# Optimization experiments

Measured on AMD Instinct MI355X. Metric: run time of the kernel, lower is better.

## Reference

```python
import jax, jax.numpy as jnp
import numpy as np

D = 1024   # embedding_dim
H = 16     # head_num
DH = D // H
STD = 0.02


def setup_inputs() -> dict:
    key = jax.random.key(0)
    ks = jax.random.split(key, 8)
    B, S = 16, 2048
    inp = {
        "hidden_states": jax.random.normal(ks[0], (B, S, D), dtype=jnp.float32),
        "attention_mask": jnp.zeros((B, 1, S), dtype=jnp.float32),
        # nn.Linear params, stored as [in, out] for direct matmul
        "Wq": jax.random.normal(ks[1], (D, D), dtype=jnp.float32) * STD,
        "bq": jnp.zeros((D,), dtype=jnp.float32),
        "Wqa": jax.random.normal(ks[2], (D, H), dtype=jnp.float32) * STD,
        "bqa": jnp.zeros((H,), dtype=jnp.float32),
        "Wk": jax.random.normal(ks[3], (D, D), dtype=jnp.float32) * STD,
        "bk": jnp.zeros((D,), dtype=jnp.float32),
        "Wka": jax.random.normal(ks[4], (D, H), dtype=jnp.float32) * STD,
        "bka": jnp.zeros((H,), dtype=jnp.float32),
        "Wt": jax.random.normal(ks[5], (D, D), dtype=jnp.float32) * STD,
        "bt": jnp.zeros((D,), dtype=jnp.float32),
    }
    return inp


def reference(hidden_states, attention_mask, Wq, bq, Wqa, bqa, Wk, bk, Wka, bka, Wt, bt):
    B, S, _ = hidden_states.shape
    scale = 1.0 / np.sqrt(DH).astype(np.float32)

    mixed_q = hidden_states @ Wq + bq          # [B,S,D]
    mixed_k = hidden_states @ Wk + bk          # [B,S,D]

    # per-head query pooling scores: [B,S,H] -> [B,H,S]
    q_score = jnp.transpose(mixed_q @ Wqa + bqa, (0, 2, 1)) * scale + attention_mask
    q_weight = jax.nn.softmax(q_score, axis=-1)                 # [B,H,S]

    q_layer = mixed_q.reshape(B, S, H, DH).transpose(0, 2, 1, 3)  # [B,H,S,dh]
    pooled_q = jnp.einsum('bhs,bhsd->bhd', q_weight, q_layer)     # [B,H,dh]
    pooled_q_flat = pooled_q.reshape(B, 1, D)                     # [B,1,D] (head-major)

    # elementwise modulate keys with pooled query (broadcast, no repeat)
    mixed_qk = mixed_k * pooled_q_flat                            # [B,S,D]

    qk_score = jnp.transpose(mixed_qk @ Wka + bka, (0, 2, 1)) * scale + attention_mask
    qk_weight = jax.nn.softmax(qk_score, axis=-1)                 # [B,H,S]

    k_layer = mixed_qk.reshape(B, S, H, DH).transpose(0, 2, 1, 3)  # [B,H,S,dh]
    pooled_k = jnp.einsum('bhs,bhsd->bhd', qk_weight, k_layer)     # [B,H,dh]

    weighted = pooled_k[:, :, None, :] * q_layer                   # [B,H,S,dh]
    weighted = weighted.transpose(0, 2, 1, 3).reshape(B, S, D)     # [B,S,D]

    return weighted @ Wt + bt + mixed_q
```

## Files before the change

### kernel.cpp

```cpp
#include <hip/hip_runtime.h>
#include <hip/hip_bf16.h>
#include <stdint.h>

#define D_ 1024
#define H_ 16
#define DH_ 64
#define S_ 2048
#define B_ 16
static constexpr float SCALE = 0.125f;

typedef __bf16 bf16_t;
typedef __bf16 bf16x8 __attribute__((ext_vector_type(8)));
typedef __bf16 bf16x4 __attribute__((ext_vector_type(4)));
typedef float  f32x4  __attribute__((ext_vector_type(4)));

__device__ __forceinline__ void llds16(const void* g, void* l) {
  __builtin_amdgcn_global_load_lds(
      (const __attribute__((address_space(1))) void*)g,
      (__attribute__((address_space(3))) void*)l, 16, 0, 0);
}

__global__ __launch_bounds__(256)
void f32_to_bf16(const float* __restrict__ src, bf16_t* __restrict__ dst) {
  size_t base = ((size_t)blockIdx.x * 256 + threadIdx.x) * 8;
  f32x4 a = *(const f32x4*)&src[base];
  f32x4 b = *(const f32x4*)&src[base + 4];
  bf16x8 o;
#pragma unroll
  for (int i = 0; i < 4; ++i) { o[i] = (bf16_t)a[i]; o[4 + i] = (bf16_t)b[i]; }
  *(bf16x8*)&dst[base] = o;
}

__global__ __launch_bounds__(256)
void transpose1024(const float* __restrict__ src, bf16_t* __restrict__ dst) {
  __shared__ bf16_t t[64][65];
  const int n0 = blockIdx.x * 64, k0 = blockIdx.y * 64;
  const int r = threadIdx.x >> 4, c4 = (threadIdx.x & 15) * 4;
#pragma unroll
  for (int p = 0; p < 4; ++p) {
    int row = p * 16 + r;
    f32x4 f = *(const f32x4*)&src[(size_t)(k0 + row) * 1024 + n0 + c4];
#pragma unroll
    for (int i = 0; i < 4; ++i) t[row][c4 + i] = (bf16_t)f[i];
  }
  __syncthreads();
#pragma unroll
  for (int p = 0; p < 4; ++p) {
    int row = p * 16 + r;
    bf16x4 v;
#pragma unroll
    for (int i = 0; i < 4; ++i) v[i] = t[c4 + i][row];
    *(bf16x4*)&dst[(size_t)(n0 + row) * 1024 + k0 + c4] = v;
  }
}

__global__ __launch_bounds__(256)
void transpose_small(const float* __restrict__ src, bf16_t* __restrict__ dst) {
  int k = blockIdx.x * 256 + threadIdx.x;
  if (k < 1024) {
#pragma unroll
    for (int h = 0; h < H_; ++h) dst[h * 1024 + k] = (bf16_t)src[k * H_ + h];
  }
}

__global__ __launch_bounds__(256)
void conv_misc(const float* bqa, const float* bka, const float* mask,
               bf16_t* obqa, bf16_t* obka, bf16_t* omask) {
  int i = blockIdx.x * 256 + threadIdx.x;
  const float* src; bf16_t* dst; int off;
  if      (i < 16)    { src = bqa;  dst = obqa;  off = i; }
  else if (i < 32)    { src = bka;  dst = obka;  off = i - 16; }
  else if (i < 32800) { src = mask; dst = omask; off = i - 32; }
  else return;
  dst[off] = (bf16_t)src[off];
}

template <int MODE>
__global__ __launch_bounds__(512, 1)
void gemm256(const bf16_t* __restrict__ A, const bf16_t* __restrict__ BT,
             const float* __restrict__ bias, void* __restrict__ Cout,
             const float* __restrict__ pscale, const bf16_t* __restrict__ resid) {
  constexpr int K = 1024;
  __shared__ __align__(16) bf16_t lds[2][2][256 * 64];
  const int tid = threadIdx.x;
  const int lane = tid & 63, wid = tid >> 6;
  const int wm = wid >> 2, wn = wid & 3;

  const int wgid = (blockIdx.x & 7) * 64 + (blockIdx.x >> 3);
  const int m0 = (wgid >> 2) * 256;
  const int n0 = (wgid & 3) * 256;

  const bf16_t* gA[4];
  const bf16_t* gB[4];
  int ldsOff[4];
#pragma unroll
  for (int i = 0; i < 4; ++i) {
    int c = i * 512 + tid;
    int r = c >> 3, j = c & 7;
    int col = ((j ^ (r & 7)) << 3);
    gA[i] = A  + (size_t)(m0 + r) * K + col;
    gB[i] = BT + (size_t)(n0 + r) * K + col;
    ldsOff[i] = c * 8;
  }

  f32x4 acc[8][4] = {};
  const int ar = lane & 15;
  const int kq = lane >> 4;

  bf16_t* curA = &lds[0][0][0]; bf16_t* curB = &lds[0][1][0];
  bf16_t* nxtA = &lds[1][0][0]; bf16_t* nxtB = &lds[1][1][0];

#pragma unroll
  for (int i = 0; i < 4; ++i) { llds16(gA[i], curA + ldsOff[i]); llds16(gB[i], curB + ldsOff[i]); }
  __syncthreads();

  for (int t = 0; t < 16; ++t) {
    const int koff = (t + 1) * 64;
#pragma unroll
    for (int q = 0; q < 4; ++q) {
      if (t < 15) {
        llds16(gA[q] + koff, nxtA + ldsOff[q]);
        llds16(gB[q] + koff, nxtB + ldsOff[q]);
      }
      const int mh = q >> 1, nh = q & 1;
      bf16x8 af[4][2], bg[2][2];
#pragma unroll
      for (int mm = 0; mm < 4; ++mm) {
        int r = wm * 128 + (mh * 4 + mm) * 16 + ar;
#pragma unroll
        for (int kk = 0; kk < 2; ++kk)
          af[mm][kk] = *(const bf16x8*)&curA[r * 64 + (((kk * 4 + kq) ^ (r & 7)) << 3)];
      }
#pragma unroll
      for (int nn = 0; nn < 2; ++nn) {
        int r = wn * 64 + (nh * 2 + nn) * 16 + ar;
#pragma unroll
        for (int kk = 0; kk < 2; ++kk)
          bg[nn][kk] = *(const bf16x8*)&curB[r * 64 + (((kk * 4 + kq) ^ (r & 7)) << 3)];
      }
      __builtin_amdgcn_s_barrier();
      __builtin_amdgcn_s_setprio(1);
#pragma unroll
      for (int mm = 0; mm < 4; ++mm)
#pragma unroll
        for (int nn = 0; nn < 2; ++nn)
#pragma unroll
          for (int kk = 0; kk < 2; ++kk)
            acc[mh * 4 + mm][nh * 2 + nn] = __builtin_amdgcn_mfma_f32_16x16x32_bf16(
                af[mm][kk], bg[nn][kk], acc[mh * 4 + mm][nh * 2 + nn], 0, 0, 0);
      __builtin_amdgcn_s_setprio(0);
      if (q < 3) __builtin_amdgcn_s_barrier();
    }
    __syncthreads();
    bf16_t* tA = curA; curA = nxtA; nxtA = tA;
    bf16_t* tB = curB; curB = nxtB; nxtB = tB;
  }

  float* st = (float*)(&lds[0][0][0]) + wid * (16 * 68);
  const int b = m0 / S_;
  const int erow = lane >> 2;
  const int ecol = (lane & 3) * 16;
  const int gcb = n0 + wn * 64;
  const int qrow = (lane >> 4) * 4;
  const int qcol = lane & 15;
  f32x4 bb[4], ps[4];
#pragma unroll
  for (int q = 0; q < 4; ++q) bb[q] = *(const f32x4*)&bias[gcb + ecol + q * 4];
  if (MODE == 1) {
#pragma unroll
    for (int q = 0; q < 4; ++q) ps[q] = *(const f32x4*)&pscale[b * D_ + gcb + ecol + q * 4];
  }
#pragma unroll
  for (int m = 0; m < 8; ++m) {
#pragma unroll
    for (int n = 0; n < 4; ++n)
#pragma unroll
      for (int j = 0; j < 4; ++j)
        st[(qrow + j) * 68 + n * 16 + qcol] = acc[m][n][j];
    asm volatile("s_waitcnt lgkmcnt(0)" ::: "memory");
    __builtin_amdgcn_sched_barrier(0);
    const int grow = m0 + wm * 128 + m * 16 + erow;
    f32x4 v[4];
#pragma unroll
    for (int q = 0; q < 4; ++q) v[q] = *(f32x4*)&st[erow * 68 + ecol + q * 4];
#pragma unroll
    for (int q = 0; q < 4; ++q)
#pragma unroll
      for (int i = 0; i < 4; ++i) v[q][i] += bb[q][i];
    if (MODE == 1) {
#pragma unroll
      for (int q = 0; q < 4; ++q)
#pragma unroll
        for (int i = 0; i < 4; ++i) v[q][i] *= ps[q][i];
    }
    if (MODE == 2) {
      bf16x8 r0 = *(const bf16x8*)&resid[(size_t)grow * D_ + gcb + ecol];
      bf16x8 r1 = *(const bf16x8*)&resid[(size_t)grow * D_ + gcb + ecol + 8];
#pragma unroll
      for (int i = 0; i < 4; ++i) { v[0][i] += (float)r0[i]; v[1][i] += (float)r0[4 + i]; }
#pragma unroll
      for (int i = 0; i < 4; ++i) { v[2][i] += (float)r1[i]; v[3][i] += (float)r1[4 + i]; }
      float* op = (float*)Cout + (size_t)grow * D_ + gcb + ecol;
#pragma unroll
      for (int q = 0; q < 4; ++q) *(f32x4*)&op[q * 4] = v[q];
    } else {
      bf16x8 o0, o1;
#pragma unroll
      for (int i = 0; i < 4; ++i) { o0[i] = (bf16_t)v[0][i]; o0[4 + i] = (bf16_t)v[1][i]; }
#pragma unroll
      for (int i = 0; i < 4; ++i) { o1[i] = (bf16_t)v[2][i]; o1[4 + i] = (bf16_t)v[3][i]; }
      bf16_t* op = (bf16_t*)Cout + (size_t)grow * D_ + gcb + ecol;
      *(bf16x8*)&op[0] = o0;
      *(bf16x8*)&op[8] = o1;
    }
  }
}

__global__ __launch_bounds__(256)
void score_kernel(const bf16_t* __restrict__ X, const bf16_t* __restrict__ WaT,
                  const bf16_t* __restrict__ ba, const bf16_t* __restrict__ mask,
                  float* __restrict__ scores) {
  const int lane = threadIdx.x & 63, wid = threadIdx.x >> 6;
  const int m0 = blockIdx.x * 64 + wid * 16;
  const int ar = lane & 15, ak = (lane >> 4) * 8;
  f32x4 acc = {};
  for (int k0 = 0; k0 < D_; k0 += 32) {
    bf16x8 a = *(const bf16x8*)&X[(size_t)(m0 + ar) * D_ + k0 + ak];
    bf16x8 b = *(const bf16x8*)&WaT[(size_t)ar * D_ + k0 + ak];
    acc = __builtin_amdgcn_mfma_f32_16x16x32_bf16(a, b, acc, 0, 0, 0);
  }
  const int h = lane & 15;
  const int srow = m0 + (lane >> 4) * 4;
  const int bb = srow / S_;
  const int s0 = srow - bb * S_;
  const float bah = (float)ba[h];
  f32x4 outv;
#pragma unroll
  for (int j = 0; j < 4; ++j)
    outv[j] = (acc[j] + bah) * SCALE + (float)mask[(size_t)bb * S_ + s0 + j];
  *(f32x4*)&scores[((size_t)(bb * H_ + h)) * S_ + s0] = outv;
}

__global__ __launch_bounds__(256)
void softmax_rows(const float* __restrict__ scores, float* __restrict__ wout) {
  __shared__ float rA[4], rB[4];
  const int tid = threadIdx.x, lane = tid & 63, wid = tid >> 6;
  const float* srow = scores + (size_t)blockIdx.x * S_;
  float* wrow = wout + (size_t)blockIdx.x * S_;
  f32x4 v0 = *(const f32x4*)&srow[tid * 4];
  f32x4 v1 = *(const f32x4*)&srow[1024 + tid * 4];
  float mx = fmaxf(fmaxf(fmaxf(v0[0], v0[1]), fmaxf(v0[2], v0[3])),
                   fmaxf(fmaxf(v1[0], v1[1]), fmaxf(v1[2], v1[3])));
#pragma unroll
  for (int o = 32; o; o >>= 1) mx = fmaxf(mx, __shfl_xor(mx, o));
  if (lane == 0) rA[wid] = mx;
  __syncthreads();
  mx = fmaxf(fmaxf(rA[0], rA[1]), fmaxf(rA[2], rA[3]));
  float sum = 0.f;
#pragma unroll
  for (int i = 0; i < 4; ++i) { v0[i] = __expf(v0[i] - mx); sum += v0[i]; }
#pragma unroll
  for (int i = 0; i < 4; ++i) { v1[i] = __expf(v1[i] - mx); sum += v1[i]; }
#pragma unroll
  for (int o = 32; o; o >>= 1) sum += __shfl_xor(sum, o);
  if (lane == 0) rB[wid] = sum;
  __syncthreads();
  sum = rB[0] + rB[1] + rB[2] + rB[3];
  const float inv = 1.0f / sum;
#pragma unroll
  for (int i = 0; i < 4; ++i) { v0[i] *= inv; v1[i] *= inv; }
  *(f32x4*)&wrow[tid * 4] = v0;
  *(f32x4*)&wrow[1024 + tid * 4] = v1;
}

__global__ __launch_bounds__(256)
void pool_partial(const bf16_t* __restrict__ X, const float* __restrict__ w,
                  float* __restrict__ partials) {
  __shared__ float sm[2][1024];
  const int tid = threadIdx.x;
  const int chunk = blockIdx.x, b = blockIdx.y;
  const int s0 = chunk * 32;
  const int dc = (tid & 127) * 8;
  const int sp = tid >> 7;
  const int h = dc >> 6;
  const float* wrow = w + ((size_t)b * H_ + h) * S_ + s0;
  const bf16_t* Xb = X + ((size_t)b * S_ + s0) * D_ + dc;
  float acc[8] = {};
  for (int s = sp; s < 32; s += 2) {
    bf16x8 xv = *(const bf16x8*)&Xb[(size_t)s * D_];
    float wt = wrow[s];
#pragma unroll
    for (int j = 0; j < 8; ++j) acc[j] += wt * (float)xv[j];
  }
#pragma unroll
  for (int j = 0; j < 8; ++j) sm[sp][dc + j] = acc[j];
  __syncthreads();
  const int d0 = tid * 4;
  f32x4 r;
#pragma unroll
  for (int j = 0; j < 4; ++j) r[j] = sm[0][d0 + j] + sm[1][d0 + j];
  *(f32x4*)&partials[((size_t)chunk * B_ + b) * D_ + d0] = r;
}

__global__ __launch_bounds__(256)
void pool_reduce(const float* __restrict__ partials, float* __restrict__ pooled) {
  const int idx = blockIdx.x * 256 + threadIdx.x;
  float s = 0.f;
#pragma unroll 8
  for (int c = 0; c < 64; ++c) s += partials[(size_t)c * (B_ * D_) + idx];
  pooled[idx] = s;
}

__global__ __launch_bounds__(256)
void weighted_kernel(const bf16_t* __restrict__ mq, const float* __restrict__ pk,
                     bf16_t* __restrict__ out) {
  size_t idx = ((size_t)blockIdx.x * 256 + threadIdx.x) * 8;
  int d0 = (int)(idx & (D_ - 1));
  int b = (int)(idx >> 21);
  bf16x8 v = *(const bf16x8*)&mq[idx];
  const float* pkb = pk + (size_t)b * D_ + d0;
  bf16x8 o;
#pragma unroll
  for (int i = 0; i < 8; ++i) o[i] = (bf16_t)((float)v[i] * pkb[i]);
  *(bf16x8*)&out[idx] = o;
}

extern "C" void kernel_launch(void* const* d_in, const int* in_sizes, int n_in,
                              void* d_out, int out_size, void* d_ws, size_t ws_size,
                              hipStream_t stream) {
  const float* hs   = (const float*)d_in[0];
  const float* mask = (const float*)d_in[1];
  const float* Wq   = (const float*)d_in[2];
  const float* bq   = (const float*)d_in[3];
  const float* Wqa  = (const float*)d_in[4];
  const float* bqa  = (const float*)d_in[5];
  const float* Wk   = (const float*)d_in[6];
  const float* bk   = (const float*)d_in[7];
  const float* Wka  = (const float*)d_in[8];
  const float* bka  = (const float*)d_in[9];
  const float* Wt   = (const float*)d_in[10];
  const float* bt   = (const float*)d_in[11];

  char* ws = (char*)d_ws;
  float*  pq    = (float*)(ws + (64u << 10));
  float*  pk    = (float*)(ws + (128u << 10));
  bf16_t* bqac  = (bf16_t*)(ws + (192u << 10));
  bf16_t* bkac  = (bf16_t*)(ws + (192u << 10) + 64);
  bf16_t* maskc = (bf16_t*)(ws + (256u << 10));
  bf16_t* WqaT  = (bf16_t*)(ws + (1u << 20));
  bf16_t* WkaT  = (bf16_t*)(ws + (1u << 20) + 32768);
  bf16_t* WqT   = (bf16_t*)(ws + (2u << 20));
  bf16_t* WkT   = (bf16_t*)(ws + (4u << 20));
  bf16_t* WtT   = (bf16_t*)(ws + (6u << 20));
  bf16_t* hsb   = (bf16_t*)(ws + (8u << 20));
  bf16_t* mq    = (bf16_t*)(ws + (8u << 20) + ((size_t)64 << 20));
  bf16_t* mqk   = (bf16_t*)(ws + (8u << 20) + ((size_t)128 << 20));
  bf16_t* wtd   = (bf16_t*)(ws + (8u << 20) + ((size_t)192 << 20));
  float* scores = (float*)(ws + (8u << 20) + ((size_t)256 << 20));
  float* wsm    = (float*)(ws + (8u << 20) + ((size_t)258 << 20));
  float* parts  = (float*)(ws + (8u << 20) + ((size_t)260 << 20));

  f32_to_bf16<<<16384, 256, 0, stream>>>(hs, hsb);
  conv_misc<<<129, 256, 0, stream>>>(bqa, bka, mask, bqac, bkac, maskc);
  transpose1024<<<dim3(16, 16), 256, 0, stream>>>(Wq, WqT);
  transpose1024<<<dim3(16, 16), 256, 0, stream>>>(Wk, WkT);
  transpose1024<<<dim3(16, 16), 256, 0, stream>>>(Wt, WtT);
  transpose_small<<<4, 256, 0, stream>>>(Wqa, WqaT);
  transpose_small<<<4, 256, 0, stream>>>(Wka, WkaT);

  gemm256<0><<<512, 512, 0, stream>>>(hsb, WqT, bq, mq, nullptr, nullptr);

  score_kernel<<<512, 256, 0, stream>>>(mq, WqaT, bqac, maskc, scores);
  softmax_rows<<<256, 256, 0, stream>>>(scores, wsm);
  pool_partial<<<dim3(64, 16), 256, 0, stream>>>(mq, wsm, parts);
  pool_reduce<<<64, 256, 0, stream>>>(parts, pq);

  gemm256<1><<<512, 512, 0, stream>>>(hsb, WkT, bk, mqk, pq, nullptr);

  score_kernel<<<512, 256, 0, stream>>>(mqk, WkaT, bkac, maskc, scores);
  softmax_rows<<<256, 256, 0, stream>>>(scores, wsm);
  pool_partial<<<dim3(64, 16), 256, 0, stream>>>(mqk, wsm, parts);
  pool_reduce<<<64, 256, 0, stream>>>(parts, pk);

  weighted_kernel<<<16384, 256, 0, stream>>>(mq, pk, wtd);

  gemm256<2><<<512, 512, 0, stream>>>(wtd, WtT, bt, d_out, nullptr, mq);
}
```

Measured before the change: 413.0 us.

## Restructure GEMM main loop with explicit vmcnt waits and k-half MFMA blocks

The GEMM inner loop now issues all global->LDS prefetches for the next k-tile up front. It waits on outstanding loads with an explicit s_waitcnt vmcnt(8) instead of a full __syncthreads, then runs a single barrier. The compute is reorganised from four quadrant sub-steps with interleaved barriers into two k-halves, each loading 8 A and 4 B fragments and issuing 32 MFMAs. This is meant to cut barrier count and let prefetch overlap compute, at the cost of higher register pressure from the larger fragment arrays. It also relies on the exact vmcnt count matching the number of outstanding loads.

Result: faster. 398.2 us (-3.6%).

```diff
diff --git a/kernel.cpp b/kernel.cpp
--- a/kernel.cpp
+++ b/kernel.cpp
@@ -112,46 +112,43 @@
 
 #pragma unroll
   for (int i = 0; i < 4; ++i) { llds16(gA[i], curA + ldsOff[i]); llds16(gB[i], curB + ldsOff[i]); }
-  __syncthreads();
 
   for (int t = 0; t < 16; ++t) {
-    const int koff = (t + 1) * 64;
-#pragma unroll
-    for (int q = 0; q < 4; ++q) {
-      if (t < 15) {
-        llds16(gA[q] + koff, nxtA + ldsOff[q]);
-        llds16(gB[q] + koff, nxtB + ldsOff[q]);
+    if (t < 15) {
+      const int koff = (t + 1) * 64;
+#pragma unroll
+      for (int i = 0; i < 4; ++i) {
+        llds16(gA[i] + koff, nxtA + ldsOff[i]);
+        llds16(gB[i] + koff, nxtB + ldsOff[i]);
       }
-      const int mh = q >> 1, nh = q & 1;
-      bf16x8 af[4][2], bg[2][2];
-#pragma unroll
-      for (int mm = 0; mm < 4; ++mm) {
-        int r = wm * 128 + (mh * 4 + mm) * 16 + ar;
-#pragma unroll
-        for (int kk = 0; kk < 2; ++kk)
-          af[mm][kk] = *(const bf16x8*)&curA[r * 64 + (((kk * 4 + kq) ^ (r & 7)) << 3)];
+      asm volatile("s_waitcnt vmcnt(8)" ::: "memory");
+    } else {
+      asm volatile("s_waitcnt vmcnt(0)" ::: "memory");
+    }
+    __builtin_amdgcn_s_barrier();
+
+#pragma unroll
+    for (int h = 0; h < 2; ++h) {
+      bf16x8 af[8], bg[4];
+#pragma unroll
+      for (int m = 0; m < 8; ++m) {
+        int r = wm * 128 + m * 16 + ar;
+        af[m] = *(const bf16x8*)&curA[r * 64 + (((h * 4 + kq) ^ (r & 7)) << 3)];
       }
 #pragma unroll
-      for (int nn = 0; nn < 2; ++nn) {
-        int r = wn * 64 + (nh * 2 + nn) * 16 + ar;
-#pragma unroll
-        for (int kk = 0; kk < 2; ++kk)
-          bg[nn][kk] = *(const bf16x8*)&curB[r * 64 + (((kk * 4 + kq) ^ (r & 7)) << 3)];
+      for (int n = 0; n < 4; ++n) {
+        int r = wn * 64 + n * 16 + ar;
+        bg[n] = *(const bf16x8*)&curB[r * 64 + (((h * 4 + kq) ^ (r & 7)) << 3)];
       }
-      __builtin_amdgcn_s_barrier();
       __builtin_amdgcn_s_setprio(1);
 #pragma unroll
-      for (int mm = 0; mm < 4; ++mm)
-#pragma unroll
-        for (int nn = 0; nn < 2; ++nn)
-#pragma unroll
-          for (int kk = 0; kk < 2; ++kk)
-            acc[mh * 4 + mm][nh * 2 + nn] = __builtin_amdgcn_mfma_f32_16x16x32_bf16(
-                af[mm][kk], bg[nn][kk], acc[mh * 4 + mm][nh * 2 + nn], 0, 0, 0);
+      for (int m = 0; m < 8; ++m)
+#pragma unroll
+        for (int n = 0; n < 4; ++n)
+          acc[m][n] = __builtin_amdgcn_mfma_f32_16x16x32_bf16(af[m], bg[n], acc[m][n], 0, 0, 0);
       __builtin_amdgcn_s_setprio(0);
-      if (q < 3) __builtin_amdgcn_s_barrier();
     }
-    __syncthreads();
+    __builtin_amdgcn_s_barrier();
     bf16_t* tA = curA; curA = nxtA; nxtA = tA;
     bf16_t* tB = curB; curB = nxtB; nxtB = tB;
   }
```
